# Performance work log

Measured on AMD Instinct MI355X. Metric: run time of the kernel, lower is better.

## Reference

```python
import jax, jax.numpy as jnp
import numpy as np

V, E, U, B, S = 32000, 512, 1024, 16, 128
BN_EPS = 1e-3  # keras BatchNormalization default


def setup_inputs() -> dict:
    key = jax.random.key(0)
    ks = jax.random.split(key, 12)
    w = 0.05  # small init keeps the relu-activated LSTM recurrence stable
    return {
        "inputs": jax.random.randint(ks[0], (B, S), 0, V),
        "enc_hidden": jax.random.normal(ks[1], (B, U), jnp.float32) * 0.1,
        "enc_cell": jax.random.normal(ks[2], (B, U), jnp.float32) * 0.1,
        "emb": jax.random.normal(ks[3], (V, E), jnp.float32) * w,
        "Wx": jax.random.normal(ks[4], (E, 4 * U), jnp.float32) * w,
        "Wh": jax.random.normal(ks[5], (U, 4 * U), jnp.float32) * w,
        "b": jnp.zeros((4 * U,), jnp.float32),
        "gamma": jnp.ones((U,), jnp.float32),
        "beta": jnp.zeros((U,), jnp.float32),
        "mov_mean": jnp.zeros((U,), jnp.float32),
        "mov_var": jnp.ones((U,), jnp.float32),
        "W1": jax.random.normal(ks[6], (U, U), jnp.float32) * w,
        "b1": jnp.zeros((U,), jnp.float32),
        "W2": jax.random.normal(ks[7], (U, V), jnp.float32) * w,
        "b2": jnp.zeros((V,), jnp.float32),
    }


def _lstm_relu(xg, mask, h0, c0, Wh):
    # xg: [S,B,4U] precomputed input gates; mask: [S,B] (mask_zero semantics)
    def step(carry, inp):
        h, c = carry
        g, m = inp
        z = g + h @ Wh  # [B,4U]
        i, f, cc, o = jnp.split(z, 4, axis=-1)  # keras gate order i,f,c,o
        i = jax.nn.sigmoid(i)
        f = jax.nn.sigmoid(f)
        o = jax.nn.sigmoid(o)
        cc = jax.nn.relu(cc)  # activation='relu' on candidate
        c_new = f * c + i * cc
        h_new = o * jax.nn.relu(c_new)  # activation='relu' on output
        m = m[:, None]
        h_new = jnp.where(m, h_new, h)  # masked step: carry state/output
        c_new = jnp.where(m, c_new, c)
        return (h_new, c_new), h_new

    (_, _), hs = jax.lax.scan(step, (h0, c0), (xg, mask))
    return hs  # [S,B,U]


def reference(inputs, enc_hidden, enc_cell, emb, Wx, Wh, b, gamma, beta,
              mov_mean, mov_var, W1, b1, W2, b2):
    x = emb[inputs]                       # [B,S,E]
    mask = (inputs != 0)                  # mask_zero=True
    xg = jnp.einsum("bse,eg->bsg", x, Wx) + b   # [B,S,4U]
    hs = _lstm_relu(xg.transpose(1, 0, 2), mask.T, enc_hidden, enc_cell, Wh)
    h = hs.transpose(1, 0, 2)             # [B,S,U]
    # BatchNorm (inference: moving statistics), Dropout is identity at inference
    hbn = (h - mov_mean) * jax.lax.rsqrt(mov_var + BN_EPS) * gamma + beta
    d1 = jax.nn.relu(hbn @ W1 + b1)       # [B,S,U]
    logits = d1 @ W2 + b2                 # [B,S,V]
    return jax.nn.softmax(logits, axis=-1)
```

## Files before the change

### kernel.cpp

```cpp
#include <hip/hip_runtime.h>
#include <hip/hip_bf16.h>
#include <stdint.h>

typedef unsigned short u16;
typedef unsigned int u32;
typedef unsigned long long u64;
typedef __attribute__((ext_vector_type(4))) float f32x4;
typedef __attribute__((ext_vector_type(8))) short s16x8;
typedef __attribute__((ext_vector_type(4))) unsigned int u32x4;

#define AT_LD(p)    __hip_atomic_load((p), __ATOMIC_RELAXED, __HIP_MEMORY_SCOPE_AGENT)
#define AT_ST(p, v) __hip_atomic_store((p), (v), __ATOMIC_RELAXED, __HIP_MEMORY_SCOPE_AGENT)
#define AT_FAA(p)   __hip_atomic_fetch_add((p), 1u, __ATOMIC_RELAXED, __HIP_MEMORY_SCOPE_AGENT)


static __device__ __forceinline__ u16 f2bf(float f) {
  union { float f; unsigned u; } v; v.f = f;
  unsigned r = v.u + 0x7FFFu + ((v.u >> 16) & 1u);
  return (u16)(r >> 16);
}

static __device__ __forceinline__ float bf2f(u16 b) {
  union { unsigned u; float f; } v; v.u = ((u32)b) << 16;
  return v.f;
}

static __device__ __forceinline__ void gload_lds16(const void* g, void* l) {
  __builtin_amdgcn_global_load_lds(
      (const __attribute__((address_space(1))) unsigned int*)(uintptr_t)g,
      (__attribute__((address_space(3))) unsigned int*)(uintptr_t)l,
      16, 0, 0);
}

static __device__ __forceinline__ int swzB(int B) {
  int pos = (B >> 4) & 127;
  int row = (B >> 11) & 15;
  int slot = (pos ^ row ^ (pos >> 3)) & 7;
  int npos = (pos & 0x78) | slot;
  return (B & ~0x7F0) | (npos << 4);
}

__global__ void prepass_kernel(const int* __restrict__ inputs,
                               const float* __restrict__ emb,
                               u16* __restrict__ xbf,
                               const float* __restrict__ Wx, u16* __restrict__ Wxt,
                               const float* __restrict__ Wh, u16* __restrict__ Wht,
                               const float* __restrict__ W1, u16* __restrict__ W1t,
                               const float* __restrict__ W2, u16* __restrict__ W2t,
                               u64* __restrict__ mb) {
  __shared__ float t[32][33];
  int b = blockIdx.x;

  if (b < 512) {
    int i = b * 256 + threadIdx.x;
    int row = i >> 6;
    int e0 = (i & 63) << 3;
    int tok = inputs[row];
    const float* src = emb + (size_t)tok * 512 + e0;
    s16x8 o;
#pragma unroll
    for (int j = 0; j < 8; ++j) o[j] = (short)f2bf(src[j]);
    *(s16x8*)(xbf + (size_t)row * 512 + e0) = o;
    return;
  }

  if (b == 39680) {
    int tq = threadIdx.x;
    if (tq < 32) {
      int bb = tq >> 1, h = tq & 1;
      u64 m = 0;
      for (int j = 0; j < 64; ++j)
        m |= (u64)(inputs[bb * 128 + h * 64 + j] != 0) << j;
      mb[tq] = m;
    }
    return;
  }

  const float* W; u16* Wt; int K, N, tt;
  if (b < 2560)      { W = Wx; Wt = Wxt; K = 512;  N = 4096;  tt = b - 512;  }
  else if (b < 6656) { W = Wh; Wt = Wht; K = 1024; N = 4096;  tt = b - 2560; }
  else if (b < 7680) { W = W1; Wt = W1t; K = 1024; N = 1024;  tt = b - 6656; }
  else               { W = W2; Wt = W2t; K = 1024; N = 32000; tt = b - 7680; }
  int ntn = N >> 5;
  int tn = tt % ntn, tk = tt / ntn;
  int n0 = tn << 5, k0 = tk << 5;
  int tx = threadIdx.x & 31, ty = threadIdx.x >> 5;
#pragma unroll
  for (int j = 0; j < 4; ++j) {
    int k = ty * 4 + j;
    t[k][tx] = W[(size_t)(k0 + k) * N + n0 + tx];
  }
  __syncthreads();
#pragma unroll
  for (int j = 0; j < 4; ++j) {
    int n = ty * 4 + j;
    Wt[(size_t)(n0 + n) * K + k0 + tx] = f2bf(t[tx][n]);
  }
}

template <int MODE>
__global__ __launch_bounds__(256)
void gemm_bf16(const u16* __restrict__ A, const u16* __restrict__ Bt,
               const float* __restrict__ bias, void* __restrict__ Cptr,
               float* __restrict__ rowsum, int M, int N, int K) {
  (void)M;
  __shared__ u16 sA[128 * 32];
  __shared__ u16 sB[128 * 32];
  const int nbn = N >> 7;
  const int nwg = gridDim.x;
  int bid = blockIdx.x;
  int q = nwg >> 3;
  int swz = (bid & 7) * q + (bid >> 3);
  int bm = swz / nbn, bn = swz % nbn;
  const int brow = bm << 7, bcol = bn << 7;

  const int tid = threadIdx.x;
  const int lane = tid & 63;
  const int wv = tid >> 6;
  const int wr = (wv >> 1) * 64, wc = (wv & 1) * 64;
  const int ln = lane & 15, kh = lane >> 4;

  const int srow = tid >> 2;
  const int kch = (tid & 3) << 3;

  f32x4 acc[4][4] = {};

  const int nk = K >> 5;
  const u16* Abase = A + (size_t)(brow + srow) * K + kch;
  const u16* Bbase = Bt + (size_t)(bcol + srow) * K + kch;
  const size_t rstride = (size_t)64 * K;
  u16* lA = sA + srow * 32 + kch;
  u16* lB = sB + srow * 32 + kch;

  for (int kt = 0; kt < nk; ++kt) {
    const int k0 = kt << 5;
    gload_lds16(Abase + k0, lA);
    gload_lds16(Abase + rstride + k0, lA + 64 * 32);
    gload_lds16(Bbase + k0, lB);
    gload_lds16(Bbase + rstride + k0, lB + 64 * 32);
    __syncthreads();
    s16x8 aF[4], bF[4];
#pragma unroll
    for (int m = 0; m < 4; ++m)
      aF[m] = *(const s16x8*)(sA + (wr + m * 16 + ln) * 32 + kh * 8);
#pragma unroll
    for (int n = 0; n < 4; ++n)
      bF[n] = *(const s16x8*)(sB + (wc + n * 16 + ln) * 32 + kh * 8);
#pragma unroll
    for (int m = 0; m < 4; ++m)
#pragma unroll
      for (int n = 0; n < 4; ++n)
        acc[m][n] = __builtin_amdgcn_mfma_f32_16x16x32_bf16(aF[m], bF[n], acc[m][n], 0, 0, 0);
    __syncthreads();
  }

  const int browq = brow + wr;
  const int bcolq = bcol + wc;

  if (MODE == 1) {
    u16* O = (u16*)Cptr;
#pragma unroll
    for (int n = 0; n < 4; ++n) {
      int gcol = bcolq + n * 16 + ln;
      float bv = bias[gcol];
#pragma unroll
      for (int m = 0; m < 4; ++m)
#pragma unroll
        for (int r = 0; r < 4; ++r) {
          int grow = browq + m * 16 + kh * 4 + r;
          float v = fmaxf(acc[m][n][r] + bv, 0.f);
          O[(size_t)grow * N + gcol] = f2bf(v);
        }
    }
  } else {
    float* O = (float*)Cptr;
    float rs[4][4] = {};
#pragma unroll
    for (int n = 0; n < 4; ++n) {
      int gcol = bcolq + n * 16 + ln;
      float bv = bias[gcol];
#pragma unroll
      for (int m = 0; m < 4; ++m)
#pragma unroll
        for (int r = 0; r < 4; ++r) {
          int grow = browq + m * 16 + kh * 4 + r;
          float v = acc[m][n][r] + bv;
          if (MODE == 2) { v = __expf(v); rs[m][r] += v; }
          O[(size_t)grow * N + gcol] = v;
        }
    }
    if (MODE == 2) {
#pragma unroll
      for (int m = 0; m < 4; ++m)
#pragma unroll
        for (int r = 0; r < 4; ++r) {
          float v = rs[m][r];
          v += __shfl_xor(v, 1);
          v += __shfl_xor(v, 2);
          v += __shfl_xor(v, 4);
          v += __shfl_xor(v, 8);
          if (ln == 0) atomicAdd(&rowsum[browq + m * 16 + kh * 4 + r], v);
        }
    }
  }
}

__global__ __launch_bounds__(512, 1)
void gemm256_exp(const u16* __restrict__ A, const u16* __restrict__ Bt,
                 const float* __restrict__ bias, u16* __restrict__ O,
                 float* __restrict__ rowsum, int M, int N, int K) {
  (void)M;
  __shared__ char lds[131072];
  const int nbn = N >> 8;
  const int nwg = gridDim.x;
  int bid = blockIdx.x;
  int q = nwg >> 3;
  int swz = (bid & 7) * q + (bid >> 3);
  int bm = swz / nbn, bn = swz % nbn;
  const int brow = bm << 8, bcol = bn << 8;

  const int tid = threadIdx.x;
  const int lane = tid & 63;
  const int wv = tid >> 6;
  const int wm = wv >> 2, wn = wv & 3;
  const int ln = lane & 15, kh = lane >> 4;

  const int nk = K >> 5;

  const u16* sbase[4];
#pragma unroll
  for (int j = 0; j < 4; ++j) {
    int cc = (j & 1) * 512 + wv * 64 + lane;
    int row = cc >> 2, pcol = cc & 3;
    int lcol = pcol ^ ((row >> 1) & 3);
    sbase[j] = (j < 2 ? A + (size_t)(brow + row) * K
                      : Bt + (size_t)(bcol + row) * K) + lcol * 8;
  }

#define STAGE256(kt, buf)                                                  \
  {                                                                        \
    char* lb = lds + (buf) * 32768 + wv * 1024;                            \
    _Pragma("unroll")                                                      \
    for (int j = 0; j < 4; ++j)                                            \
      gload_lds16(sbase[j] + (kt) * 32, lb + j * 8192);                    \
  }

  f32x4 acc[8][4] = {};

  STAGE256(0, 0);
  STAGE256(1, 1);
  asm volatile("s_waitcnt vmcnt(4)" ::: "memory");
  __syncthreads();

  const char* Ab = lds + (size_t)(wm * 128) * 64;
  const char* Bb = lds + 16384 + (size_t)(wn * 64) * 64;
  const int cswz = (kh ^ ((ln >> 1) & 3)) * 16 + ln * 64;

  for (int t = 0; t < nk; ++t) {
    const int boff = (t & 3) * 32768;
    if (t + 2 < nk) STAGE256(t + 2, (t + 2) & 3);
    s16x8 aF[8], bF[4];
#pragma unroll
    for (int m = 0; m < 8; ++m)
      aF[m] = *(const s16x8*)(Ab + boff + m * 1024 + cswz);
#pragma unroll
    for (int n = 0; n < 4; ++n)
      bF[n] = *(const s16x8*)(Bb + boff + n * 1024 + cswz);
    __builtin_amdgcn_s_setprio(1);
#pragma unroll
    for (int m = 0; m < 8; ++m)
#pragma unroll
      for (int n = 0; n < 4; ++n)
        acc[m][n] = __builtin_amdgcn_mfma_f32_16x16x32_bf16(aF[m], bF[n], acc[m][n], 0, 0, 0);
    __builtin_amdgcn_s_setprio(0);
    if (t + 2 < nk)
      asm volatile("s_waitcnt vmcnt(4)" ::: "memory");
    else
      asm volatile("s_waitcnt vmcnt(0)" ::: "memory");
    if (t < nk - 1) __syncthreads();
  }

  const int browq = brow + wm * 128;
  const int bcolq = bcol + wn * 64;
  float rs[8][4] = {};
#pragma unroll
  for (int n = 0; n < 4; ++n) {
    int gcol = bcolq + n * 16 + ln;
    float bv = bias[gcol];
#pragma unroll
    for (int m = 0; m < 8; ++m)
#pragma unroll
      for (int r = 0; r < 4; ++r) {
        float v = __expf(acc[m][n][r] + bv);
        rs[m][r] += v;
        O[(size_t)(browq + m * 16 + kh * 4 + r) * N + gcol] = f2bf(v);
      }
  }
#pragma unroll
  for (int m = 0; m < 8; ++m)
#pragma unroll
    for (int r = 0; r < 4; ++r) {
      float v = rs[m][r];
      v += __shfl_xor(v, 1);
      v += __shfl_xor(v, 2);
      v += __shfl_xor(v, 4);
      v += __shfl_xor(v, 8);
      if (ln == 0) atomicAdd(&rowsum[browq + m * 16 + kh * 4 + r], v);
    }
#undef STAGE256
}

__global__ __launch_bounds__(512, 1)
void lstm_kernel(const float* __restrict__ xg,
                 const u16* __restrict__ Wht,
                 const u64* __restrict__ maskb,
                 const float* __restrict__ ench, const float* __restrict__ encc,
                 const float* __restrict__ gamma, const float* __restrict__ beta,
                 const float* __restrict__ mmean, const float* __restrict__ mvar,
                 u32* __restrict__ hbuf32,
                 u16* __restrict__ hbn,
                 u32* __restrict__ cnt) {
  __shared__ char hA[32 * 1024];

  const int wg = blockIdx.x;
  const int u0 = wg << 5;
  const int tid = threadIdx.x;
  const int lane = tid & 63;
  const int wv = tid >> 6;
  const int ln = lane & 15, khq = lane >> 4;

  const int g = ln & 3;
  const int unit = u0 + wv * 4 + (ln >> 2);

  u32x4 bWq[32];
  {
    const u16* wrow = Wht + (size_t)(g * 1024 + unit) * 1024 + khq * 8;
#pragma unroll
    for (int kt = 0; kt < 32; ++kt) {
      const u16* pp = wrow + kt * 32;
      asm volatile("global_load_dwordx4 %0, %1, off" : "=v"(bWq[kt]) : "v"(pp));
    }
    asm volatile("s_waitcnt vmcnt(0)" ::: "memory");
  }

  float cellR[4], holdR[4], xgr[4];
  u64 mA[4], mB[4];
  const float bn_s = gamma[unit] * rsqrtf(mvar[unit] + 1e-3f);
  const float bn_b = beta[unit] - mmean[unit] * bn_s;
  const size_t bstride = (size_t)128 * 4096;
  const float* xbase = xg + (size_t)(khq * 4) * bstride + g * 1024 + unit;
#pragma unroll
  for (int r = 0; r < 4; ++r) {
    int batch = khq * 4 + r;
    cellR[r] = encc[batch * 1024 + unit];
    holdR[r] = ench[batch * 1024 + unit];
    mA[r] = maskb[batch * 2];
    mB[r] = maskb[batch * 2 + 1];
  }
#pragma unroll
  for (int r = 0; r < 4; ++r) {
    u32 w = (u32)f2bf(holdR[r]);
    u32 pw = (u32)__shfl_xor((int)w, 4);
    if ((ln & 7) == 0) {
      int batch = khq * 4 + r;
      AT_ST((u32*)((char*)hbuf32 + batch * 2048 + unit * 2), (w & 0xFFFFu) | (pw << 16));
    }
  }
#pragma unroll
  for (int r = 0; r < 4; ++r) xgr[r] = xbase[r * bstride];
  asm volatile("s_waitcnt vmcnt(0)" ::: "memory");
  __syncthreads();
  if (tid == 0) {
    u32 oldv = AT_FAA(cnt);
    if (oldv != 31u) {
      int c = 0;
      while (AT_LD((const u32*)cnt) < 32u) {
        __builtin_amdgcn_s_sleep(1);
        if (++c > (1 << 18)) break;
      }
    }
  }
  __syncthreads();

  for (int s = 0; s < 128; ++s) {
    u64 st[8];
    {
      const u64* base = (const u64*)((const char*)hbuf32 + (s & 1) * 32768) + tid;
#pragma unroll
      for (int k = 0; k < 8; ++k) {
        const u64* pp = base + k * 512;
        asm volatile("global_load_dwordx2 %0, %1, off sc0 sc1" : "=v"(st[k]) : "v"(pp));
      }
      asm volatile("s_waitcnt vmcnt(0)" ::: "memory");
      __builtin_amdgcn_sched_barrier(0);
#pragma unroll
      for (int k = 0; k < 8; ++k)
        *(u64*)(hA + swzB((tid + k * 512) * 8)) = st[k];
    }
    __syncthreads();

    f32x4 acc0 = {0.f, 0.f, 0.f, 0.f};
    f32x4 acc1 = {0.f, 0.f, 0.f, 0.f};
#pragma unroll
    for (int kt = 0; kt < 32; kt += 2) {
      s16x8 a0 = *(const s16x8*)(hA + swzB(ln * 2048 + kt * 64 + khq * 16));
      acc0 = __builtin_amdgcn_mfma_f32_16x16x32_bf16(
          a0, __builtin_bit_cast(s16x8, bWq[kt]), acc0, 0, 0, 0);
      s16x8 a1 = *(const s16x8*)(hA + swzB(ln * 2048 + (kt + 1) * 64 + khq * 16));
      acc1 = __builtin_amdgcn_mfma_f32_16x16x32_bf16(
          a1, __builtin_bit_cast(s16x8, bWq[kt + 1]), acc1, 0, 0, 0);
    }
    f32x4 accs = acc0 + acc1;

    u32 bnpair[4];
    {
      u16 hbb[4], hbnb[4];
#pragma unroll
      for (int r = 0; r < 4; ++r) {
        float z = accs[r] + xgr[r];
        float sig = 1.f / (1.f + __expf(-z));
        float val = (g == 2) ? fmaxf(z, 0.f) : sig;
        float v1 = __shfl_xor(val, 1);
        float v2 = __shfl_xor(val, 2);
        float v3 = __shfl_xor(val, 3);
        float cnew = v1 * cellR[r] + val * v2;
        float hnew = v3 * fmaxf(cnew, 0.f);
        u64 mm = (s < 64) ? mA[r] : mB[r];
        if (!((mm >> (s & 63)) & 1)) { cnew = cellR[r]; hnew = holdR[r]; }
        cellR[r] = cnew;
        holdR[r] = hnew;
        hbb[r] = f2bf(hnew);
        hbnb[r] = f2bf(hnew * bn_s + bn_b);
      }
#pragma unroll
      for (int r = 0; r < 4; ++r) {
        u32 w = (u32)hbb[r] | ((u32)hbnb[r] << 16);
        u32 pw = (u32)__shfl_xor((int)w, 4);
        u32 hpair = (w & 0xFFFFu) | ((pw & 0xFFFFu) << 16);
        bnpair[r] = (w >> 16) | (pw & 0xFFFF0000u);
        if (s < 127 && (ln & 7) == 0) {
          int batch = khq * 4 + r;
          AT_ST((u32*)((char*)hbuf32 + ((s + 1) & 1) * 32768 + batch * 2048 + unit * 2), hpair);
        }
      }
    }

    if (s < 127) {
      asm volatile("s_waitcnt vmcnt(0)" ::: "memory");
      __syncthreads();
      u32 oldv = 0xFFFFFFFFu;
      if (tid == 0) oldv = AT_FAA(cnt);
      if ((ln & 7) == 0) {
#pragma unroll
        for (int r = 0; r < 4; ++r) {
          int batch = khq * 4 + r;
          *(u32*)((char*)hbn + (size_t)(batch * 128 + s) * 2048 + unit * 2) = bnpair[r];
        }
      }
      {
        const float* xb = xbase + (size_t)(s + 1) * 4096;
#pragma unroll
        for (int r = 0; r < 4; ++r) xgr[r] = xb[r * bstride];
      }
      if (tid == 0) {
        const u32 target = (u32)(s + 2) * 32u;
        if (oldv != target - 1u) {
          int c = 0;
          while (AT_LD((const u32*)cnt) < target) {
            __builtin_amdgcn_s_sleep(1);
            if (++c > (1 << 18)) break;
          }
        }
      }
      __syncthreads();
    } else if ((ln & 7) == 0) {
#pragma unroll
      for (int r = 0; r < 4; ++r) {
        int batch = khq * 4 + r;
        *(u32*)((char*)hbn + (size_t)(batch * 128 + s) * 2048 + unit * 2) = bnpair[r];
      }
    }
  }
}


__global__ void scale_kernel(float* __restrict__ out, const float* __restrict__ rs) {
  const int total4 = 16384000;
  for (int i = blockIdx.x * 256 + threadIdx.x; i < total4; i += gridDim.x * 256) {
    float4* p = (float4*)out + i;
    float4 v = *p;
    int row = i / 8000;
    float sF = 1.0f / rs[row];
    v.x *= sF; v.y *= sF; v.z *= sF; v.w *= sF;
    *p = v;
  }
}

__global__ __launch_bounds__(256)
void scale_bf_kernel(float* __restrict__ out, const u16* __restrict__ e,
                     const float* __restrict__ rs) {
  const int row = blockIdx.x;
  const float sF = 1.0f / rs[row];
  const s16x8* src = (const s16x8*)(e + (size_t)row * 32000);
  float4* dst = (float4*)(out + (size_t)row * 32000);
  for (int i = threadIdx.x; i < 4000; i += 256) {
    s16x8 v = src[i];
    float4 o0, o1;
    o0.x = bf2f((u16)v[0]) * sF; o0.y = bf2f((u16)v[1]) * sF;
    o0.z = bf2f((u16)v[2]) * sF; o0.w = bf2f((u16)v[3]) * sF;
    o1.x = bf2f((u16)v[4]) * sF; o1.y = bf2f((u16)v[5]) * sF;
    o1.z = bf2f((u16)v[6]) * sF; o1.w = bf2f((u16)v[7]) * sF;
    dst[2 * i] = o0;
    dst[2 * i + 1] = o1;
  }
}


extern "C" void kernel_launch(void* const* d_in, const int* in_sizes, int n_in,
                              void* d_out, int out_size, void* d_ws, size_t ws_size,
                              hipStream_t stream) {
  (void)in_sizes; (void)n_in; (void)out_size;
  const int*   inputs = (const int*)d_in[0];
  const float* ench   = (const float*)d_in[1];
  const float* encc   = (const float*)d_in[2];
  const float* emb    = (const float*)d_in[3];
  const float* Wx     = (const float*)d_in[4];
  const float* Wh     = (const float*)d_in[5];
  const float* bb     = (const float*)d_in[6];
  const float* gamma  = (const float*)d_in[7];
  const float* beta   = (const float*)d_in[8];
  const float* mmean  = (const float*)d_in[9];
  const float* mvar   = (const float*)d_in[10];
  const float* W1     = (const float*)d_in[11];
  const float* b1     = (const float*)d_in[12];
  const float* W2     = (const float*)d_in[13];
  const float* b2     = (const float*)d_in[14];
  float* out = (float*)d_out;

  char* p = (char*)d_ws;
  u32*   cnt    = (u32*)(p + 0);
  float* rowsum = (float*)(p + 1024);
  u64*   maskb  = (u64*)(p + 10240);
  u32*   hbuf32 = (u32*)(p + 16384);
  size_t off = 81920;
  u16*   xbf  = (u16*)(p + off);     off += (size_t)2048 * 512 * 2;
  u16*   Wxt  = (u16*)(p + off);     off += (size_t)4096 * 512 * 2;
  u16*   Wht  = (u16*)(p + off);     off += (size_t)4096 * 1024 * 2;
  u16*   W1t  = (u16*)(p + off);     off += (size_t)1024 * 1024 * 2;
  u16*   W2t  = (u16*)(p + off);     off += (size_t)32000 * 1024 * 2;
  float* xg   = (float*)(p + off);   off += (size_t)2048 * 4096 * 4;
  u16*   hbn  = (u16*)(p + off);     off += (size_t)2048 * 1024 * 2;
  u16*   d1   = (u16*)(p + off);     off += (size_t)2048 * 1024 * 2;
  size_t off_base = off;
  u16*   expbf = (u16*)(p + off);    off += (size_t)2048 * 32000 * 2;
  if (ws_size < off_base) return;
  const bool bf16path = (ws_size >= off);

  hipMemsetAsync(d_ws, 0, 9216, stream);

  prepass_kernel<<<39681, 256, 0, stream>>>(inputs, emb, xbf, Wx, Wxt, Wh, Wht,
                                            W1, W1t, W2, W2t, maskb);

  gemm_bf16<0><<<16 * 32, 256, 0, stream>>>(xbf, Wxt, bb, xg, nullptr, 2048, 4096, 512);

  lstm_kernel<<<32, 512, 0, stream>>>(xg, Wht, maskb, ench, encc, gamma, beta,
                                      mmean, mvar, hbuf32, hbn, cnt);

  gemm_bf16<1><<<16 * 8, 256, 0, stream>>>(hbn, W1t, b1, d1, nullptr, 2048, 1024, 1024);

  if (bf16path) {
    gemm256_exp<<<8 * 125, 512, 0, stream>>>(d1, W2t, b2, expbf, rowsum, 2048, 32000, 1024);
    scale_bf_kernel<<<2048, 256, 0, stream>>>(out, expbf, rowsum);
  } else {
    gemm_bf16<2><<<16 * 250, 256, 0, stream>>>(d1, W2t, b2, out, rowsum, 2048, 32000, 1024);
    scale_kernel<<<2048, 256, 0, stream>>>(out, rowsum);
  }
}
```

Before: 887.1 us.

## Overlap W1/W2 bf16 transpose with LSTM recurrence via extra blocks

Moves the fp32-to-bf16 transpose of W1 and W2 out of the prepass kernel. It now runs in 16512 extra blocks appended to the LSTM launch, each handling two 32x32 tiles using the LSTM kernel's shared-memory buffer. The 32-block recurrent LSTM leaves most CUs idle, and this conversion is meant to fill them so that heavy memory traffic hides under the serial recurrence. The risk is that the extra blocks share CUs and memory bandwidth with the latency-sensitive LSTM blocks, and the scheme relies on the 32 LSTM blocks being dispatched first for its cross-block synchronization.

```diff
diff --git a/kernel.cpp b/kernel.cpp
--- a/kernel.cpp
+++ b/kernel.cpp
@@ -45,8 +45,6 @@
                                u16* __restrict__ xbf,
                                const float* __restrict__ Wx, u16* __restrict__ Wxt,
                                const float* __restrict__ Wh, u16* __restrict__ Wht,
-                               const float* __restrict__ W1, u16* __restrict__ W1t,
-                               const float* __restrict__ W2, u16* __restrict__ W2t,
                                u64* __restrict__ mb) {
   __shared__ float t[32][33];
   int b = blockIdx.x;
@@ -64,7 +62,7 @@
     return;
   }
 
-  if (b == 39680) {
+  if (b == 6656) {
     int tq = threadIdx.x;
     if (tq < 32) {
       int bb = tq >> 1, h = tq & 1;
@@ -77,10 +75,8 @@
   }
 
   const float* W; u16* Wt; int K, N, tt;
-  if (b < 2560)      { W = Wx; Wt = Wxt; K = 512;  N = 4096;  tt = b - 512;  }
-  else if (b < 6656) { W = Wh; Wt = Wht; K = 1024; N = 4096;  tt = b - 2560; }
-  else if (b < 7680) { W = W1; Wt = W1t; K = 1024; N = 1024;  tt = b - 6656; }
-  else               { W = W2; Wt = W2t; K = 1024; N = 32000; tt = b - 7680; }
+  if (b < 2560) { W = Wx; Wt = Wxt; K = 512;  N = 4096; tt = b - 512;  }
+  else          { W = Wh; Wt = Wht; K = 1024; N = 4096; tt = b - 2560; }
   int ntn = N >> 5;
   int tn = tt % ntn, tk = tt / ntn;
   int n0 = tn << 5, k0 = tk << 5;
@@ -319,8 +315,35 @@
                  const float* __restrict__ mmean, const float* __restrict__ mvar,
                  u32* __restrict__ hbuf32,
                  u16* __restrict__ hbn,
-                 u32* __restrict__ cnt) {
+                 u32* __restrict__ cnt,
+                 const float* __restrict__ W1, u16* __restrict__ W1t,
+                 const float* __restrict__ W2, u16* __restrict__ W2t) {
   __shared__ char hA[32 * 1024];
+
+  if (blockIdx.x >= 32) {
+    int tt2 = (blockIdx.x - 32) * 2 + (threadIdx.x >> 8);
+    const float* W; u16* Wt; int K, N, tt;
+    if (tt2 < 1024) { W = W1; Wt = W1t; K = 1024; N = 1024;  tt = tt2; }
+    else            { W = W2; Wt = W2t; K = 1024; N = 32000; tt = tt2 - 1024; }
+    int ntn = N >> 5;
+    int tn = tt % ntn, tk = tt / ntn;
+    int n0 = tn << 5, k0 = tk << 5;
+    float (*t)[33] = (float(*)[33])(hA + (threadIdx.x >> 8) * 4352);
+    int t256 = threadIdx.x & 255;
+    int tx = t256 & 31, ty = t256 >> 5;
+#pragma unroll
+    for (int j = 0; j < 4; ++j) {
+      int k = ty * 4 + j;
+      t[k][tx] = W[(size_t)(k0 + k) * N + n0 + tx];
+    }
+    __syncthreads();
+#pragma unroll
+    for (int j = 0; j < 4; ++j) {
+      int n = ty * 4 + j;
+      Wt[(size_t)(n0 + n) * K + k0 + tx] = f2bf(t[tx][n]);
+    }
+    return;
+  }
 
   const int wg = blockIdx.x;
   const int u0 = wg << 5;
@@ -558,13 +581,13 @@
 
   hipMemsetAsync(d_ws, 0, 9216, stream);
 
-  prepass_kernel<<<39681, 256, 0, stream>>>(inputs, emb, xbf, Wx, Wxt, Wh, Wht,
-                                            W1, W1t, W2, W2t, maskb);
+  prepass_kernel<<<6657, 256, 0, stream>>>(inputs, emb, xbf, Wx, Wxt, Wh, Wht, maskb);
 
   gemm_bf16<0><<<16 * 32, 256, 0, stream>>>(xbf, Wxt, bb, xg, nullptr, 2048, 4096, 512);
 
-  lstm_kernel<<<32, 512, 0, stream>>>(xg, Wht, maskb, ench, encc, gamma, beta,
-                                      mmean, mvar, hbuf32, hbn, cnt);
+  lstm_kernel<<<32 + 16512, 512, 0, stream>>>(xg, Wht, maskb, ench, encc, gamma, beta,
+                                              mmean, mvar, hbuf32, hbn, cnt,
+                                              W1, W1t, W2, W2t);
 
   gemm_bf16<1><<<16 * 8, 256, 0, stream>>>(hbn, W1t, b1, d1, nullptr, 2048, 1024, 1024);
 
```

After: 846.6 us. 1.05x faster.
